# Kernel optimization log

Measured on AMD Instinct MI355X. Metric: run time of the kernel, lower is better.

## Reference

```python
import jax, jax.numpy as jnp
import numpy as np

F = 200        # factors
D = 64         # first attention layer width
P = 512        # positive items per user
R = 49         # regions per image (7x7)
FEAT = 2048    # feature channels
NU = 100000    # num users
NI = 50000     # num items


def _glorot(key, shape):
    lim = float(np.sqrt(6.0 / (shape[0] + shape[-1])))
    return jax.random.uniform(key, shape, jnp.float32, -lim, lim)


def setup_inputs() -> dict:
    key = jax.random.key(0)
    ks = jax.random.split(key, 20)
    inp = {
        "f_u_i_pos": jax.random.normal(ks[0], (1, P, R, FEAT), jnp.float32),
        "Gu": 0.01 * jax.random.normal(ks[1], (NU, F), jnp.float32),
        "Gi": 0.01 * jax.random.normal(ks[2], (NI, F), jnp.float32),
        "Pi": 0.01 * jax.random.normal(ks[3], (NI, F), jnp.float32),
        # component-level attention weights
        "Wc0_u": _glorot(ks[4], (F, D)),
        "Wc0_i": _glorot(ks[5], (FEAT, D)),
        "bc0": _glorot(ks[6], (D,)),
        "Wc1": _glorot(ks[7], (D, 1)),
        "bc1": _glorot(ks[8], (1,)),
        # item-level attention weights
        "Wi0_u": _glorot(ks[9], (F, D)),
        "Wi0_iv": _glorot(ks[10], (F, D)),
        "Wi0_ip": _glorot(ks[11], (F, D)),
        "Wi0_ix": _glorot(ks[12], (FEAT, D)),
        "bi0": _glorot(ks[13], (D,)),
        "Wi1": _glorot(ks[14], (D, 1)),
        "bi1": _glorot(ks[15], (1,)),
        "user": 7,
        "item": 3,
        "user_pos": jax.random.randint(ks[16], (1, P), 0, NI, jnp.int32),
    }
    return inp


def reference(f_u_i_pos, Gu, Gi, Pi,
              Wc0_u, Wc0_i, bc0, Wc1, bc1,
              Wi0_u, Wi0_iv, Wi0_ip, Wi0_ix, bi0, Wi1, bi1,
              user, item, user_pos):
    g_u = Gu[user]                 # [F]
    gamma_i = Gi[item]             # [F]
    p_i_item = Pi[item]            # [F]
    g_pos = Gi[user_pos]           # [1, P, F]
    p_pos = Pi[user_pos]           # [1, P, F]

    # ---- component-level attention (over R=49 regions) ----
    # logits: [1, P, R, D]
    b = jax.nn.relu(f_u_i_pos @ Wc0_i + (g_u @ Wc0_u) + bc0)
    b = b @ Wc1 + bc1              # [1, P, R, 1]
    b = jax.nn.softmax(b, axis=2)  # softmax over regions
    all_x = jnp.sum(b * f_u_i_pos, axis=2)  # [1, P, FEAT]

    # ---- item-level attention (over P positive items) ----
    a = jax.nn.relu((g_u @ Wi0_u)
                    + g_pos @ Wi0_iv
                    + p_pos @ Wi0_ip
                    + all_x @ Wi0_ix
                    + bi0)         # [1, P, D]
    a = a @ Wi1 + bi1              # [1, P, 1]
    a = jax.nn.softmax(a, axis=1)  # softmax over positive items (TF axis=2 of [1,1,P,1])
    all_a = jnp.sum(a * p_pos, axis=1)  # [1, F]

    g_u_p = g_u + all_a[0]         # [F]
    xui = jnp.sum(g_u_p * gamma_i) # scalar
    return (xui, g_u, gamma_i, p_i_item)
```

## Files before the change

### kernel.cpp

```cpp
#include <hip/hip_runtime.h>
#include <hip/hip_bf16.h>
#include <stdint.h>

#define P_CNT 512
#define R_CNT 49
#define FEAT  2048
#define FDIM  200
#define DDIM  64
#define KC2   64
#define NCH2  (FEAT / KC2)
#define MROWS (P_CNT * R_CNT)
#define LOG2E 1.44269504f

typedef __bf16 bf16;
typedef bf16  bf16x8 __attribute__((ext_vector_type(8)));
typedef float f32x4  __attribute__((ext_vector_type(4)));

#define WS_U0    0
#define WS_UI0   256
#define WS_LIT   512
#define WS_LOG   4096
#define WS_PART  104448
#define WS_WCT   131072
#define WS_ALLX  393216

__device__ __forceinline__ void gl_lds16(const void* g, void* l) {
  auto gp = reinterpret_cast<const uint32_t __attribute__((address_space(1)))*>(
      reinterpret_cast<uintptr_t>(g));
  auto lp = reinterpret_cast<uint32_t __attribute__((address_space(3)))*>(
      reinterpret_cast<uintptr_t>(l));
  __builtin_amdgcn_global_load_lds(gp, lp, 16, 0, 0);
}

__global__ __launch_bounds__(256) void k_prep(
    const float* __restrict__ Gu, const float* __restrict__ Gi, const float* __restrict__ Pi,
    const float* __restrict__ Wc0u, const float* __restrict__ bc0,
    const float* __restrict__ Wi0u, const float* __restrict__ bi0,
    const int* __restrict__ user, const int* __restrict__ item,
    float* __restrict__ out, float* __restrict__ ws)
{
  __shared__ float red[2][4][64];
  int tid = threadIdx.x;
  int d = tid & 63, q = tid >> 6;
  int us = user[0], it = item[0];
  const float* gu = Gu + (size_t)us * FDIM;
  float s0 = 0.f, s1 = 0.f;
#pragma unroll 5
  for (int f = q * 50; f < q * 50 + 50; ++f) {
    float g = gu[f];
    s0 += g * Wc0u[f * 64 + d];
    s1 += g * Wi0u[f * 64 + d];
  }
  red[0][q][d] = s0;
  red[1][q][d] = s1;
  __syncthreads();
  if (tid < 64) {
    ws[WS_U0 / 4 + tid] = red[0][0][tid] + red[0][1][tid] + red[0][2][tid] + red[0][3][tid] + bc0[tid];
  } else if (tid < 128) {
    int dd = tid - 64;
    ws[WS_UI0 / 4 + dd] = red[1][0][dd] + red[1][1][dd] + red[1][2][dd] + red[1][3][dd] + bi0[dd];
  }
  for (int i = tid; i < FDIM; i += 256) {
    out[1 + i]   = gu[i];
    out[201 + i] = Gi[(size_t)it * FDIM + i];
    out[401 + i] = Pi[(size_t)it * FDIM + i];
  }
}

__global__ __launch_bounds__(256) void k_wt(const float* __restrict__ Wci, bf16* __restrict__ wct)
{
  int g = blockIdx.x * 256 + threadIdx.x;
  int d = g & 63;
  int c0 = (g >> 6) * 8;
  bf16 tmp[8];
#pragma unroll
  for (int i = 0; i < 8; ++i) tmp[i] = (bf16)Wci[(size_t)(c0 + i) * 64 + d];
  *(bf16x8*)(wct + (size_t)d * FEAT + c0) = *(bf16x8*)tmp;
}

__global__ __launch_bounds__(256) void k_gemm(
    const float* __restrict__ f, const bf16* __restrict__ wct,
    const float* __restrict__ ws_u0, const float* __restrict__ Wc1,
    float* __restrict__ logits)
{
  __shared__ __align__(16) float Af[2][64 * KC2];
  __shared__ __align__(16) bf16  Wt[2][64 * KC2];

  const int tid  = threadIdx.x;
  const int wave = tid >> 6;
  const int lane = tid & 63;
  const int cl   = lane & 15;
  const int g4   = lane >> 4;

  const size_t row0 = (size_t)blockIdx.x * 64;
  const char* fb = (const char*)(f + row0 * FEAT);
  const char* wb = (const char*)wct;

  float u0c[4], w1c[4];
#pragma unroll
  for (int n = 0; n < 4; ++n) {
    u0c[n] = ws_u0[n * 16 + cl];
    w1c[n] = Wc1[n * 16 + cl];
  }
  f32x4 acc[4];
#pragma unroll
  for (int n = 0; n < 4; ++n) acc[n] = (f32x4){0.f, 0.f, 0.f, 0.f};

  const int arow = wave * 16 + cl;
  const int asw  = (arow & 7) << 4;

  auto STAGE = [&](int b, int kc) {
    const int kc0 = kc * KC2;
    char* afb = (char*)Af[b];
    char* wtb = (char*)Wt[b];
#pragma unroll
    for (int ii = 0; ii < 4; ++ii) {
      int iss = wave * 4 + ii;
      int r   = 4 * iss + (lane >> 4);
      int boff = ((lane & 15) * 16) ^ ((r & 7) << 4);
      gl_lds16(fb + (size_t)r * (FEAT * 4) + kc0 * 4 + boff, afb + iss * 1024);
    }
#pragma unroll
    for (int ii = 0; ii < 2; ++ii) {
      int iss = wave * 2 + ii;
      int r   = 8 * iss + (lane >> 3);
      int boff = ((lane & 7) * 16) ^ ((r & 7) << 4);
      gl_lds16(wb + (size_t)r * (FEAT * 2) + kc0 * 2 + boff, wtb + iss * 1024);
    }
  };

  auto COMPUTE = [&](int b) {
    char* afb = (char*)Af[b];
    char* wtb = (char*)Wt[b];
#pragma unroll
    for (int ks = 0; ks < KC2 / 32; ++ks) {
      int kb = ks * 128 + g4 * 32;
      const float4 a0 = *(const float4*)(afb + arow * 256 + ((kb)      ^ asw));
      const float4 a1 = *(const float4*)(afb + arow * 256 + ((kb + 16) ^ asw));
      bf16x8 afr;
      afr[0] = (bf16)a0.x; afr[1] = (bf16)a0.y; afr[2] = (bf16)a0.z; afr[3] = (bf16)a0.w;
      afr[4] = (bf16)a1.x; afr[5] = (bf16)a1.y; afr[6] = (bf16)a1.z; afr[7] = (bf16)a1.w;
      int kbb = ks * 64 + g4 * 16;
#pragma unroll
      for (int n = 0; n < 4; ++n) {
        int col = n * 16 + cl;
        bf16x8 bfr = *(const bf16x8*)(wtb + col * 128 + (kbb ^ ((col & 7) << 4)));
        acc[n] = __builtin_amdgcn_mfma_f32_16x16x32_bf16(afr, bfr, acc[n], 0, 0, 0);
      }
    }
  };

  STAGE(0, 0);
  __syncthreads();
  int cur = 0;
  for (int kc = 0; kc < NCH2; ++kc) {
    if (kc + 1 < NCH2) STAGE(cur ^ 1, kc + 1);
    COMPUTE(cur);
    __syncthreads();
    cur ^= 1;
  }

#pragma unroll
  for (int j = 0; j < 4; ++j) {
    float s = 0.f;
#pragma unroll
    for (int n = 0; n < 4; ++n) {
      float v = acc[n][j] + u0c[n];
      v = fmaxf(v, 0.f);
      s += v * w1c[n];
    }
    s += __shfl_xor(s, 1);
    s += __shfl_xor(s, 2);
    s += __shfl_xor(s, 4);
    s += __shfl_xor(s, 8);
    if (cl == 0) logits[row0 + wave * 16 + g4 * 4 + j] = s;
  }
}

__global__ __launch_bounds__(256) void k_wsum(
    const float* __restrict__ f, const float* __restrict__ logits,
    float* __restrict__ allx)
{
  __shared__ float lg[R_CNT];
  const int tid = threadIdx.x;
  const int p   = blockIdx.x;
  if (tid < R_CNT) lg[tid] = logits[p * R_CNT + tid];
  __syncthreads();

  float m = -1e30f;
  for (int r = 0; r < R_CNT; ++r) m = fmaxf(m, lg[r]);
  float s = 0.f;
  for (int r = 0; r < R_CNT; ++r) s += exp2f((lg[r] - m) * LOG2E);
  float inv = 1.f / s;

  float a8[8];
#pragma unroll
  for (int i = 0; i < 8; ++i) a8[i] = 0.f;
  const float* fp = f + (size_t)p * R_CNT * FEAT + tid * 8;
  for (int r = 0; r < R_CNT; ++r) {
    float w = exp2f((lg[r] - m) * LOG2E);
    float4 x0 = *(const float4*)(fp + (size_t)r * FEAT);
    float4 x1 = *(const float4*)(fp + (size_t)r * FEAT + 4);
    a8[0] += w * x0.x; a8[1] += w * x0.y; a8[2] += w * x0.z; a8[3] += w * x0.w;
    a8[4] += w * x1.x; a8[5] += w * x1.y; a8[6] += w * x1.z; a8[7] += w * x1.w;
  }
  float* op = allx + (size_t)p * FEAT + tid * 8;
  float4 o0 = {a8[0] * inv, a8[1] * inv, a8[2] * inv, a8[3] * inv};
  float4 o1 = {a8[4] * inv, a8[5] * inv, a8[6] * inv, a8[7] * inv};
  *(float4*)op = o0;
  *(float4*)(op + 4) = o1;
}

__global__ __launch_bounds__(256) void k_item(
    const float* __restrict__ allx, const float* __restrict__ Gi, const float* __restrict__ Pi,
    const float* __restrict__ Wiv, const float* __restrict__ Wip, const float* __restrict__ Wix,
    const float* __restrict__ ws_ui0, const float* __restrict__ Wi1,
    const int* __restrict__ upos, float* __restrict__ lit)
{
  __shared__ __align__(16) float ax[2 * FEAT];
  __shared__ float gp[2][FDIM];
  __shared__ float pp[2][FDIM];
  __shared__ float zr[4][2][64];
  int tid = threadIdx.x;
  int p0 = blockIdx.x * 2;

#pragma unroll
  for (int i = 0; i < 4; ++i) {
    int j = i * 256 + tid;
    *(float4*)(ax + 4 * j) = *(const float4*)(allx + (size_t)p0 * FEAT + 4 * j);
  }
  int i0 = upos[p0], i1 = upos[p0 + 1];
  if (tid < FDIM) {
    gp[0][tid] = Gi[(size_t)i0 * FDIM + tid];
    gp[1][tid] = Gi[(size_t)i1 * FDIM + tid];
    pp[0][tid] = Pi[(size_t)i0 * FDIM + tid];
    pp[1][tid] = Pi[(size_t)i1 * FDIM + tid];
  }
  __syncthreads();

  int d = tid & 63, q = tid >> 6;
  float acc0 = 0.f, acc1 = 0.f;
  for (int c = q * 512; c < q * 512 + 512; c += 4) {
    float w0 = Wix[(size_t)(c + 0) * 64 + d];
    float w1 = Wix[(size_t)(c + 1) * 64 + d];
    float w2 = Wix[(size_t)(c + 2) * 64 + d];
    float w3 = Wix[(size_t)(c + 3) * 64 + d];
    float4 aa = *(const float4*)(ax + c);
    float4 bb = *(const float4*)(ax + FEAT + c);
    acc0 += aa.x * w0 + aa.y * w1 + aa.z * w2 + aa.w * w3;
    acc1 += bb.x * w0 + bb.y * w1 + bb.z * w2 + bb.w * w3;
  }
  for (int ff = q * 50; ff < q * 50 + 50; ++ff) {
    float wv = Wiv[(size_t)ff * 64 + d];
    float wp2 = Wip[(size_t)ff * 64 + d];
    acc0 += gp[0][ff] * wv + pp[0][ff] * wp2;
    acc1 += gp[1][ff] * wv + pp[1][ff] * wp2;
  }
  zr[q][0][d] = acc0;
  zr[q][1][d] = acc1;
  __syncthreads();
  if (tid < 128) {
    int pq = tid >> 6, dd = tid & 63;
    float z = zr[0][pq][dd] + zr[1][pq][dd] + zr[2][pq][dd] + zr[3][pq][dd] + ws_ui0[dd];
    z = fmaxf(z, 0.f);
    float t = z * Wi1[dd];
    t += __shfl_xor(t, 1);  t += __shfl_xor(t, 2);  t += __shfl_xor(t, 4);
    t += __shfl_xor(t, 8);  t += __shfl_xor(t, 16); t += __shfl_xor(t, 32);
    if (dd == 0) lit[p0 + pq] = t;
  }
}

__global__ __launch_bounds__(256) void k_fina(
    const float* __restrict__ lit, const int* __restrict__ upos,
    const float* __restrict__ Pi, float* __restrict__ part)
{
  __shared__ float la[P_CNT];
  __shared__ float red[4][FDIM];
  int tid = threadIdx.x;
  la[tid] = lit[tid];
  la[tid + 256] = lit[tid + 256];
  __syncthreads();
  float m = -1e30f;
  for (int i = 0; i < P_CNT; ++i) m = fmaxf(m, la[i]);
  float s = 0.f;
  for (int i = 0; i < P_CNT; ++i) s += exp2f((la[i] - m) * LOG2E);
  float inv = 1.f / s;

  int w = tid >> 6, lane = tid & 63;
  float a4[4] = {0.f, 0.f, 0.f, 0.f};
#pragma unroll
  for (int i = 0; i < 4; ++i) {
    int pg = blockIdx.x * 16 + w * 4 + i;
    float ap = exp2f((la[pg] - m) * LOG2E) * inv;
    const float* row = Pi + (size_t)upos[pg] * FDIM;
#pragma unroll
    for (int k = 0; k < 4; ++k) {
      int ff = lane + k * 64;
      if (ff < FDIM) a4[k] += ap * row[ff];
    }
  }
#pragma unroll
  for (int k = 0; k < 4; ++k) {
    int ff = lane + k * 64;
    if (ff < FDIM) red[w][ff] = a4[k];
  }
  __syncthreads();
  if (tid < FDIM)
    part[blockIdx.x * FDIM + tid] = red[0][tid] + red[1][tid] + red[2][tid] + red[3][tid];
}

__global__ __launch_bounds__(256) void k_finb(
    const float* __restrict__ part, const float* __restrict__ Gu, const float* __restrict__ Gi,
    const int* __restrict__ user, const int* __restrict__ item,
    float* __restrict__ out)
{
  __shared__ float pr[256];
  __shared__ float wred[4];
  int tid = threadIdx.x;
  int us = user[0], it = item[0];
  float v = 0.f;
  if (tid < FDIM) {
    float alla = 0.f;
#pragma unroll
    for (int b = 0; b < 32; ++b) alla += part[b * FDIM + tid];
    float gup = Gu[(size_t)us * FDIM + tid] + alla;
    v = gup * Gi[(size_t)it * FDIM + tid];
  }
  pr[tid] = v;
  __syncthreads();
  v = pr[tid];
  v += __shfl_xor(v, 1);  v += __shfl_xor(v, 2);  v += __shfl_xor(v, 4);
  v += __shfl_xor(v, 8);  v += __shfl_xor(v, 16); v += __shfl_xor(v, 32);
  int w = tid >> 6;
  if ((tid & 63) == 0) wred[w] = v;
  __syncthreads();
  if (tid == 0) out[0] = wred[0] + wred[1] + wred[2] + wred[3];
}

extern "C" void kernel_launch(void* const* d_in, const int* in_sizes, int n_in,
                              void* d_out, int out_size, void* d_ws, size_t ws_size,
                              hipStream_t stream)
{
  const float* f    = (const float*)d_in[0];
  const float* Gu   = (const float*)d_in[1];
  const float* Gi   = (const float*)d_in[2];
  const float* Pi   = (const float*)d_in[3];
  const float* Wc0u = (const float*)d_in[4];
  const float* Wc0i = (const float*)d_in[5];
  const float* bc0  = (const float*)d_in[6];
  const float* Wc1  = (const float*)d_in[7];
  const float* Wi0u = (const float*)d_in[9];
  const float* Wiv  = (const float*)d_in[10];
  const float* Wip  = (const float*)d_in[11];
  const float* Wix  = (const float*)d_in[12];
  const float* bi0  = (const float*)d_in[13];
  const float* Wi1  = (const float*)d_in[14];
  const int* user   = (const int*)d_in[16];
  const int* item   = (const int*)d_in[17];
  const int* upos   = (const int*)d_in[18];

  float* out  = (float*)d_out;
  char*  ws   = (char*)d_ws;
  float* u0   = (float*)(ws + WS_U0);
  float* ui0  = (float*)(ws + WS_UI0);
  float* lit  = (float*)(ws + WS_LIT);
  float* logi = (float*)(ws + WS_LOG);
  float* part = (float*)(ws + WS_PART);
  bf16*  wct  = (bf16*)(ws + WS_WCT);
  float* allx = (float*)(ws + WS_ALLX);

  hipLaunchKernelGGL(k_prep, dim3(1),   dim3(256), 0, stream, Gu, Gi, Pi, Wc0u, bc0, Wi0u, bi0, user, item, out, (float*)ws);
  hipLaunchKernelGGL(k_wt,   dim3(64),  dim3(256), 0, stream, Wc0i, wct);
  hipLaunchKernelGGL(k_gemm, dim3(MROWS / 64), dim3(256), 0, stream, f, wct, u0, Wc1, logi);
  hipLaunchKernelGGL(k_wsum, dim3(P_CNT), dim3(256), 0, stream, f, logi, allx);
  hipLaunchKernelGGL(k_item, dim3(P_CNT / 2), dim3(256), 0, stream, allx, Gi, Pi, Wiv, Wip, Wix, ui0, Wi1, upos, lit);
  hipLaunchKernelGGL(k_fina, dim3(32),  dim3(256), 0, stream, lit, upos, Pi, part);
  hipLaunchKernelGGL(k_finb, dim3(1),   dim3(256), 0, stream, part, Gu, Gi, user, item, out);
}
```

Measured before the change: 478.6 us.

## Fuse region GEMM with softmax-weighted sum per item and merge tail kernels

Each block of the GEMM now covers one positive item's 49 regions and computes the logits, the softmax and the weighted feature sum in the same block. The second pass over that item's features then reads data the block just loaded, which should mostly hit cache, and the logits buffer round-trip disappears. The prep and weight-transpose kernels are merged into a single launch. The final reduction is also rewritten as a dot product of Pi rows with gamma, accumulated into out[0] with atomicAdd, cutting the launch count from seven to four. The cost is that 64-row MFMA tiles now hold only 49 valid rows, so about a quarter of the matrix work is wasted, and the atomic ordering makes the result non-deterministic.

```diff
diff --git a/kernel.cpp b/kernel.cpp
--- a/kernel.cpp
+++ b/kernel.cpp
@@ -6,11 +6,11 @@
 #define R_CNT 49
 #define FEAT  2048
 #define FDIM  200
-#define DDIM  64
 #define KC2   64
 #define NCH2  (FEAT / KC2)
-#define MROWS (P_CNT * R_CNT)
 #define LOG2E 1.44269504f
+#define AISS  13
+#define ABUF  (AISS * 1024)
 
 typedef __bf16 bf16;
 typedef bf16  bf16x8 __attribute__((ext_vector_type(8)));
@@ -19,10 +19,8 @@
 #define WS_U0    0
 #define WS_UI0   256
 #define WS_LIT   512
-#define WS_LOG   4096
-#define WS_PART  104448
-#define WS_WCT   131072
-#define WS_ALLX  393216
+#define WS_WCT   4096
+#define WS_ALLX  266240
 
 __device__ __forceinline__ void gl_lds16(const void* g, void* l) {
   auto gp = reinterpret_cast<const uint32_t __attribute__((address_space(1)))*>(
@@ -32,68 +30,76 @@
   __builtin_amdgcn_global_load_lds(gp, lp, 16, 0, 0);
 }
 
-__global__ __launch_bounds__(256) void k_prep(
+__global__ __launch_bounds__(256) void k_init(
     const float* __restrict__ Gu, const float* __restrict__ Gi, const float* __restrict__ Pi,
     const float* __restrict__ Wc0u, const float* __restrict__ bc0,
     const float* __restrict__ Wi0u, const float* __restrict__ bi0,
+    const float* __restrict__ Wci,
     const int* __restrict__ user, const int* __restrict__ item,
-    float* __restrict__ out, float* __restrict__ ws)
-{
-  __shared__ float red[2][4][64];
+    float* __restrict__ out, float* __restrict__ ws, bf16* __restrict__ wct)
+{
   int tid = threadIdx.x;
-  int d = tid & 63, q = tid >> 6;
-  int us = user[0], it = item[0];
-  const float* gu = Gu + (size_t)us * FDIM;
-  float s0 = 0.f, s1 = 0.f;
+  if (blockIdx.x == 0) {
+    __shared__ float red[2][4][64];
+    __shared__ float wred[4];
+    int d = tid & 63, q = tid >> 6;
+    int us = user[0], it = item[0];
+    const float* gu = Gu + (size_t)us * FDIM;
+    float s0 = 0.f, s1 = 0.f;
 #pragma unroll 5
-  for (int f = q * 50; f < q * 50 + 50; ++f) {
-    float g = gu[f];
-    s0 += g * Wc0u[f * 64 + d];
-    s1 += g * Wi0u[f * 64 + d];
-  }
-  red[0][q][d] = s0;
-  red[1][q][d] = s1;
-  __syncthreads();
-  if (tid < 64) {
-    ws[WS_U0 / 4 + tid] = red[0][0][tid] + red[0][1][tid] + red[0][2][tid] + red[0][3][tid] + bc0[tid];
-  } else if (tid < 128) {
-    int dd = tid - 64;
-    ws[WS_UI0 / 4 + dd] = red[1][0][dd] + red[1][1][dd] + red[1][2][dd] + red[1][3][dd] + bi0[dd];
-  }
-  for (int i = tid; i < FDIM; i += 256) {
-    out[1 + i]   = gu[i];
-    out[201 + i] = Gi[(size_t)it * FDIM + i];
-    out[401 + i] = Pi[(size_t)it * FDIM + i];
-  }
-}
-
-__global__ __launch_bounds__(256) void k_wt(const float* __restrict__ Wci, bf16* __restrict__ wct)
-{
-  int g = blockIdx.x * 256 + threadIdx.x;
-  int d = g & 63;
-  int c0 = (g >> 6) * 8;
-  bf16 tmp[8];
-#pragma unroll
-  for (int i = 0; i < 8; ++i) tmp[i] = (bf16)Wci[(size_t)(c0 + i) * 64 + d];
-  *(bf16x8*)(wct + (size_t)d * FEAT + c0) = *(bf16x8*)tmp;
-}
-
-__global__ __launch_bounds__(256) void k_gemm(
+    for (int f2 = q * 50; f2 < q * 50 + 50; ++f2) {
+      float g = gu[f2];
+      s0 += g * Wc0u[f2 * 64 + d];
+      s1 += g * Wi0u[f2 * 64 + d];
+    }
+    red[0][q][d] = s0;
+    red[1][q][d] = s1;
+    float pv = (tid < FDIM) ? gu[tid] * Gi[(size_t)it * FDIM + tid] : 0.f;
+    pv += __shfl_xor(pv, 1);  pv += __shfl_xor(pv, 2);  pv += __shfl_xor(pv, 4);
+    pv += __shfl_xor(pv, 8);  pv += __shfl_xor(pv, 16); pv += __shfl_xor(pv, 32);
+    if (d == 0) wred[q] = pv;
+    __syncthreads();
+    if (tid < 64) {
+      ws[WS_U0 / 4 + tid] = red[0][0][tid] + red[0][1][tid] + red[0][2][tid] + red[0][3][tid] + bc0[tid];
+    } else if (tid < 128) {
+      int dd = tid - 64;
+      ws[WS_UI0 / 4 + dd] = red[1][0][dd] + red[1][1][dd] + red[1][2][dd] + red[1][3][dd] + bi0[dd];
+    } else if (tid == 128) {
+      out[0] = wred[0] + wred[1] + wred[2] + wred[3];
+    }
+    for (int i = tid; i < FDIM; i += 256) {
+      out[1 + i]   = gu[i];
+      out[201 + i] = Gi[(size_t)it * FDIM + i];
+      out[401 + i] = Pi[(size_t)it * FDIM + i];
+    }
+  } else {
+    int g = (blockIdx.x - 1) * 256 + tid;
+    int d = g & 63;
+    int c0 = (g >> 6) * 8;
+    bf16 tmp[8];
+#pragma unroll
+    for (int i = 0; i < 8; ++i) tmp[i] = (bf16)Wci[(size_t)(c0 + i) * 64 + d];
+    *(bf16x8*)(wct + (size_t)d * FEAT + c0) = *(bf16x8*)tmp;
+  }
+}
+
+__global__ __launch_bounds__(256) void k_comp(
     const float* __restrict__ f, const bf16* __restrict__ wct,
     const float* __restrict__ ws_u0, const float* __restrict__ Wc1,
-    float* __restrict__ logits)
-{
-  __shared__ __align__(16) float Af[2][64 * KC2];
-  __shared__ __align__(16) bf16  Wt[2][64 * KC2];
+    float* __restrict__ allx)
+{
+  __shared__ __align__(16) char AfB[2][ABUF];
+  __shared__ __align__(16) bf16 Wt[2][64 * KC2];
+  __shared__ float lg[64];
 
   const int tid  = threadIdx.x;
   const int wave = tid >> 6;
   const int lane = tid & 63;
   const int cl   = lane & 15;
   const int g4   = lane >> 4;
-
-  const size_t row0 = (size_t)blockIdx.x * 64;
-  const char* fb = (const char*)(f + row0 * FEAT);
+  const int p    = blockIdx.x;
+
+  const char* fb = (const char*)(f + (size_t)p * R_CNT * FEAT);
   const char* wb = (const char*)wct;
 
   float u0c[4], w1c[4];
@@ -111,14 +117,17 @@
 
   auto STAGE = [&](int b, int kc) {
     const int kc0 = kc * KC2;
-    char* afb = (char*)Af[b];
+    char* afb = AfB[b];
     char* wtb = (char*)Wt[b];
 #pragma unroll
     for (int ii = 0; ii < 4; ++ii) {
-      int iss = wave * 4 + ii;
-      int r   = 4 * iss + (lane >> 4);
-      int boff = ((lane & 15) * 16) ^ ((r & 7) << 4);
-      gl_lds16(fb + (size_t)r * (FEAT * 4) + kc0 * 4 + boff, afb + iss * 1024);
+      int iss = wave + 4 * ii;
+      if (iss < AISS) {
+        int r  = 4 * iss + (lane >> 4);
+        int rs = r < R_CNT ? r : (R_CNT - 1);
+        int boff = ((lane & 15) * 16) ^ ((r & 7) << 4);
+        gl_lds16(fb + (size_t)rs * (FEAT * 4) + kc0 * 4 + boff, afb + iss * 1024);
+      }
     }
 #pragma unroll
     for (int ii = 0; ii < 2; ++ii) {
@@ -130,7 +139,7 @@
   };
 
   auto COMPUTE = [&](int b) {
-    char* afb = (char*)Af[b];
+    char* afb = AfB[b];
     char* wtb = (char*)Wt[b];
 #pragma unroll
     for (int ks = 0; ks < KC2 / 32; ++ks) {
@@ -173,18 +182,8 @@
     s += __shfl_xor(s, 2);
     s += __shfl_xor(s, 4);
     s += __shfl_xor(s, 8);
-    if (cl == 0) logits[row0 + wave * 16 + g4 * 4 + j] = s;
-  }
-}
-
-__global__ __launch_bounds__(256) void k_wsum(
-    const float* __restrict__ f, const float* __restrict__ logits,
-    float* __restrict__ allx)
-{
-  __shared__ float lg[R_CNT];
-  const int tid = threadIdx.x;
-  const int p   = blockIdx.x;
-  if (tid < R_CNT) lg[tid] = logits[p * R_CNT + tid];
+    if (cl == 0) lg[wave * 16 + g4 * 4 + j] = s;
+  }
   __syncthreads();
 
   float m = -1e30f;
@@ -192,21 +191,24 @@
   float s = 0.f;
   for (int r = 0; r < R_CNT; ++r) s += exp2f((lg[r] - m) * LOG2E);
   float inv = 1.f / s;
+  __syncthreads();
+  if (tid < R_CNT) lg[tid] = exp2f((lg[tid] - m) * LOG2E) * inv;
+  __syncthreads();
 
   float a8[8];
 #pragma unroll
   for (int i = 0; i < 8; ++i) a8[i] = 0.f;
   const float* fp = f + (size_t)p * R_CNT * FEAT + tid * 8;
   for (int r = 0; r < R_CNT; ++r) {
-    float w = exp2f((lg[r] - m) * LOG2E);
+    float w = lg[r];
     float4 x0 = *(const float4*)(fp + (size_t)r * FEAT);
     float4 x1 = *(const float4*)(fp + (size_t)r * FEAT + 4);
     a8[0] += w * x0.x; a8[1] += w * x0.y; a8[2] += w * x0.z; a8[3] += w * x0.w;
     a8[4] += w * x1.x; a8[5] += w * x1.y; a8[6] += w * x1.z; a8[7] += w * x1.w;
   }
   float* op = allx + (size_t)p * FEAT + tid * 8;
-  float4 o0 = {a8[0] * inv, a8[1] * inv, a8[2] * inv, a8[3] * inv};
-  float4 o1 = {a8[4] * inv, a8[5] * inv, a8[6] * inv, a8[7] * inv};
+  float4 o0 = {a8[0], a8[1], a8[2], a8[3]};
+  float4 o1 = {a8[4], a8[5], a8[6], a8[7]};
   *(float4*)op = o0;
   *(float4*)(op + 4) = o1;
 }
@@ -270,71 +272,60 @@
   }
 }
 
-__global__ __launch_bounds__(256) void k_fina(
+__global__ __launch_bounds__(256) void k_fin(
     const float* __restrict__ lit, const int* __restrict__ upos,
-    const float* __restrict__ Pi, float* __restrict__ part)
+    const float* __restrict__ Pi, const float* __restrict__ Gi,
+    const int* __restrict__ item, float* __restrict__ out)
 {
   __shared__ float la[P_CNT];
-  __shared__ float red[4][FDIM];
-  int tid = threadIdx.x;
-  la[tid] = lit[tid];
-  la[tid + 256] = lit[tid + 256];
-  __syncthreads();
-  float m = -1e30f;
-  for (int i = 0; i < P_CNT; ++i) m = fmaxf(m, la[i]);
-  float s = 0.f;
-  for (int i = 0; i < P_CNT; ++i) s += exp2f((la[i] - m) * LOG2E);
-  float inv = 1.f / s;
-
-  int w = tid >> 6, lane = tid & 63;
-  float a4[4] = {0.f, 0.f, 0.f, 0.f};
+  __shared__ float rmax[4];
+  __shared__ float rsum[4];
+  __shared__ float rloc[4];
+  int tid = threadIdx.x, w = tid >> 6, lane = tid & 63;
+  float v0 = lit[tid], v1 = lit[tid + 256];
+  la[tid] = v0;
+  la[tid + 256] = v1;
+  float mx = fmaxf(v0, v1);
+  mx = fmaxf(mx, __shfl_xor(mx, 1));  mx = fmaxf(mx, __shfl_xor(mx, 2));
+  mx = fmaxf(mx, __shfl_xor(mx, 4));  mx = fmaxf(mx, __shfl_xor(mx, 8));
+  mx = fmaxf(mx, __shfl_xor(mx, 16)); mx = fmaxf(mx, __shfl_xor(mx, 32));
+  if (lane == 0) rmax[w] = mx;
+  __syncthreads();
+  float m = fmaxf(fmaxf(rmax[0], rmax[1]), fmaxf(rmax[2], rmax[3]));
+  float e = exp2f((v0 - m) * LOG2E) + exp2f((v1 - m) * LOG2E);
+  e += __shfl_xor(e, 1);  e += __shfl_xor(e, 2);  e += __shfl_xor(e, 4);
+  e += __shfl_xor(e, 8);  e += __shfl_xor(e, 16); e += __shfl_xor(e, 32);
+  if (lane == 0) rsum[w] = e;
+  __syncthreads();
+  float inv = 1.f / (rsum[0] + rsum[1] + rsum[2] + rsum[3]);
+
+  int it = item[0];
+  const float* gamma = Gi + (size_t)it * FDIM;
+  float g[4];
+#pragma unroll
+  for (int k = 0; k < 4; ++k) {
+    int ff = lane + 64 * k;
+    g[k] = (ff < FDIM) ? gamma[ff] : 0.f;
+  }
+  float local = 0.f;
 #pragma unroll
   for (int i = 0; i < 4; ++i) {
     int pg = blockIdx.x * 16 + w * 4 + i;
+    const float* row = Pi + (size_t)upos[pg] * FDIM;
+    float d = 0.f;
+#pragma unroll
+    for (int k = 0; k < 4; ++k) {
+      int ff = lane + 64 * k;
+      if (ff < FDIM) d += row[ff] * g[k];
+    }
+    d += __shfl_xor(d, 1);  d += __shfl_xor(d, 2);  d += __shfl_xor(d, 4);
+    d += __shfl_xor(d, 8);  d += __shfl_xor(d, 16); d += __shfl_xor(d, 32);
     float ap = exp2f((la[pg] - m) * LOG2E) * inv;
-    const float* row = Pi + (size_t)upos[pg] * FDIM;
-#pragma unroll
-    for (int k = 0; k < 4; ++k) {
-      int ff = lane + k * 64;
-      if (ff < FDIM) a4[k] += ap * row[ff];
-    }
-  }
-#pragma unroll
-  for (int k = 0; k < 4; ++k) {
-    int ff = lane + k * 64;
-    if (ff < FDIM) red[w][ff] = a4[k];
-  }
-  __syncthreads();
-  if (tid < FDIM)
-    part[blockIdx.x * FDIM + tid] = red[0][tid] + red[1][tid] + red[2][tid] + red[3][tid];
-}
-
-__global__ __launch_bounds__(256) void k_finb(
-    const float* __restrict__ part, const float* __restrict__ Gu, const float* __restrict__ Gi,
-    const int* __restrict__ user, const int* __restrict__ item,
-    float* __restrict__ out)
-{
-  __shared__ float pr[256];
-  __shared__ float wred[4];
-  int tid = threadIdx.x;
-  int us = user[0], it = item[0];
-  float v = 0.f;
-  if (tid < FDIM) {
-    float alla = 0.f;
-#pragma unroll
-    for (int b = 0; b < 32; ++b) alla += part[b * FDIM + tid];
-    float gup = Gu[(size_t)us * FDIM + tid] + alla;
-    v = gup * Gi[(size_t)it * FDIM + tid];
-  }
-  pr[tid] = v;
-  __syncthreads();
-  v = pr[tid];
-  v += __shfl_xor(v, 1);  v += __shfl_xor(v, 2);  v += __shfl_xor(v, 4);
-  v += __shfl_xor(v, 8);  v += __shfl_xor(v, 16); v += __shfl_xor(v, 32);
-  int w = tid >> 6;
-  if ((tid & 63) == 0) wred[w] = v;
-  __syncthreads();
-  if (tid == 0) out[0] = wred[0] + wred[1] + wred[2] + wred[3];
+    local += ap * d;
+  }
+  if (lane == 0) rloc[w] = local;
+  __syncthreads();
+  if (tid == 0) atomicAdd(out, rloc[0] + rloc[1] + rloc[2] + rloc[3]);
 }
 
 extern "C" void kernel_launch(void* const* d_in, const int* in_sizes, int n_in,
@@ -364,16 +355,13 @@
   float* u0   = (float*)(ws + WS_U0);
   float* ui0  = (float*)(ws + WS_UI0);
   float* lit  = (float*)(ws + WS_LIT);
-  float* logi = (float*)(ws + WS_LOG);
-  float* part = (float*)(ws + WS_PART);
   bf16*  wct  = (bf16*)(ws + WS_WCT);
   float* allx = (float*)(ws + WS_ALLX);
 
-  hipLaunchKernelGGL(k_prep, dim3(1),   dim3(256), 0, stream, Gu, Gi, Pi, Wc0u, bc0, Wi0u, bi0, user, item, out, (float*)ws);
-  hipLaunchKernelGGL(k_wt,   dim3(64),  dim3(256), 0, stream, Wc0i, wct);
-  hipLaunchKernelGGL(k_gemm, dim3(MROWS / 64), dim3(256), 0, stream, f, wct, u0, Wc1, logi);
-  hipLaunchKernelGGL(k_wsum, dim3(P_CNT), dim3(256), 0, stream, f, logi, allx);
-  hipLaunchKernelGGL(k_item, dim3(P_CNT / 2), dim3(256), 0, stream, allx, Gi, Pi, Wiv, Wip, Wix, ui0, Wi1, upos, lit);
-  hipLaunchKernelGGL(k_fina, dim3(32),  dim3(256), 0, stream, lit, upos, Pi, part);
-  hipLaunchKernelGGL(k_finb, dim3(1),   dim3(256), 0, stream, part, Gu, Gi, user, item, out);
-}
+  hipLaunchKernelGGL(k_init, dim3(65),    dim3(256), 0, stream,
+                     Gu, Gi, Pi, Wc0u, bc0, Wi0u, bi0, Wc0i, user, item, out, (float*)ws, wct);
+  hipLaunchKernelGGL(k_comp, dim3(P_CNT), dim3(256), 0, stream, f, wct, u0, Wc1, allx);
+  hipLaunchKernelGGL(k_item, dim3(P_CNT / 2), dim3(256), 0, stream,
+                     allx, Gi, Pi, Wiv, Wip, Wix, ui0, Wi1, upos, lit);
+  hipLaunchKernelGGL(k_fin,  dim3(32),    dim3(256), 0, stream, lit, upos, Pi, Gi, item, out);
+}
```

New measurement: 432.8 us. 1.11x faster.
